# Performance work log

Hardware: AMD Instinct MI355X
Metric: run time of the kernel (lower is better)

The kernel has to match this reference:

```python
import jax, jax.numpy as jnp
import numpy as np

NUM_HEADS = 32
HEAD_DIM = 64  # C = 3 * NUM_HEADS * HEAD_DIM = 6144
SCALE = NUM_HEADS ** (-0.5)


def setup_inputs() -> dict:
    key = jax.random.key(0)
    B, N, C = 4, 4096, 3 * NUM_HEADS * HEAD_DIM
    x = jax.random.normal(key, (B, N, C), dtype=jnp.float32)
    return {"x": x}


def reference(x):
    B, N, C = x.shape
    # (B, N, 3, H, d) -> (3, B, H, N, d)
    qkv = x.reshape(B, N, 3, NUM_HEADS, HEAD_DIM).transpose(2, 0, 3, 1, 4)
    q, k, v = qkv[0], qkv[1], qkv[2]
    q = q * SCALE
    # kv = k^T @ v : (B, H, d, d)
    kv = jnp.einsum('bhnd,bhne->bhde', k, v)
    kv = jax.nn.softmax(kv, axis=-1)  # dropout p=0.0 -> identity
    # attn = q @ kv^T : (B, H, N, d)
    attn = jnp.einsum('bhnd,bhed->bhne', q, kv)
    # (B, H, N, d) -> (B, N, H*d)
    out = attn.transpose(0, 2, 1, 3).reshape(B, N, NUM_HEADS * HEAD_DIM)
    return out
```

## Files before the change

kernel.cpp:

```cpp
#include <hip/hip_runtime.h>
#include <math.h>


#define NN 4096
#define CC 6144
#define QSCALE 0.17677669529663687f
#define NCHUNK 8

typedef __attribute__((ext_vector_type(8))) short bf16x8;
typedef __attribute__((ext_vector_type(4))) float f32x4;

static __device__ __forceinline__ unsigned short f2bf(float f) {
  unsigned u = __float_as_uint(f);
  u = (u + 0x7FFFu + ((u >> 16) & 1u)) >> 16;
  return (unsigned short)u;
}

__global__ __launch_bounds__(256, 4) void k1_kv_accum(const float* __restrict__ x,
                                                      float* __restrict__ ws1) {
  __shared__ float lds[2][4096];

  const int bid = blockIdx.x;
  const int bh = bid >> 3;
  const int chunk = bid & (NCHUNK - 1);
  const int b = bh >> 5, h = bh & 31;
  const int t = threadIdx.x;
  const int lane = t & 63;
  const int w = t >> 6;

  const long long row0 = (long long)b * NN + (long long)chunk * 512;
  const float* kbase = x + row0 * CC + 2048 + h * 64;
  const float* kl = kbase + (lane & 3) * CC + (lane >> 2) + w * 16;
  const float* vl = kl + 2048;

#define K1_STAGE(sb, bbv)                                                                 \
  do {                                                                                    \
    const float* kp_ = kl + (sb) * 32 * CC;                                               \
    const float* vp_ = vl + (sb) * 32 * CC;                                               \
    _Pragma("unroll") for (int r_ = 0; r_ < 2; ++r_)                                      \
    _Pragma("unroll") for (int sub_ = 0; sub_ < 4; ++sub_) {                              \
      const int ro_ = (sub_ * 8 + r_ * 4) * CC;                                           \
      const int li_ = w * 512 + r_ * 256 + sub_ * 64;                                     \
      __builtin_amdgcn_global_load_lds(                                                   \
          (const __attribute__((address_space(1))) void*)(kp_ + ro_),                     \
          (__attribute__((address_space(3))) void*)&lds[(bbv)][li_], 4, 0, 0);            \
      __builtin_amdgcn_global_load_lds(                                                   \
          (const __attribute__((address_space(1))) void*)(vp_ + ro_),                     \
          (__attribute__((address_space(3))) void*)&lds[(bbv)][2048 + li_], 4, 0, 0);     \
    }                                                                                     \
  } while (0)

#define K1_FRAG(bbv, baseidx, hi8, lo8)                                                   \
  do {                                                                                    \
    const float4 f0_ = *(const float4*)&lds[(bbv)][(baseidx) + lane * 4];                 \
    const float4 f1_ = *(const float4*)&lds[(bbv)][(baseidx) + 256 + lane * 4];           \
    const float ff_[8] = {f0_.x, f0_.y, f0_.z, f0_.w, f1_.x, f1_.y, f1_.z, f1_.w};        \
    _Pragma("unroll") for (int e_ = 0; e_ < 8; ++e_) {                                    \
      const unsigned u_ = __float_as_uint(ff_[e_]);                                       \
      hi8[e_] = (short)(u_ >> 16);       \
      const float lof_ = ff_[e_] - __uint_as_float(u_ & 0xFFFF0000u);                     \
      lo8[e_] = (short)(__float_as_uint(lof_) >> 16);                                     \
    }                                                                                     \
  } while (0)

  f32x4 acc[2][2];
#pragma unroll
  for (int i2 = 0; i2 < 2; ++i2)
#pragma unroll
    for (int j2 = 0; j2 < 2; ++j2) acc[i2][j2] = (f32x4){0.f, 0.f, 0.f, 0.f};

  const int mt0 = (w & 1) * 2;
  const int nt0 = (w >> 1) * 2;

  K1_STAGE(0, 0);
  asm volatile("s_waitcnt vmcnt(0)" ::: "memory");
  __syncthreads();

  for (int s = 0; s < 16; ++s) {
    const int bb = s & 1;
    if (s + 1 < 16) K1_STAGE(s + 1, bb ^ 1);

    bf16x8 ah[2], al[2], bh8[2], bl8[2];
#pragma unroll
    for (int i2 = 0; i2 < 2; ++i2) K1_FRAG(bb, (mt0 + i2) * 512, ah[i2], al[i2]);
#pragma unroll
    for (int j2 = 0; j2 < 2; ++j2) K1_FRAG(bb, 2048 + (nt0 + j2) * 512, bh8[j2], bl8[j2]);

#pragma unroll
    for (int i2 = 0; i2 < 2; ++i2)
#pragma unroll
      for (int j2 = 0; j2 < 2; ++j2) {
        acc[i2][j2] = __builtin_amdgcn_mfma_f32_16x16x32_bf16(ah[i2], bh8[j2], acc[i2][j2], 0, 0, 0);
        acc[i2][j2] = __builtin_amdgcn_mfma_f32_16x16x32_bf16(ah[i2], bl8[j2], acc[i2][j2], 0, 0, 0);
        acc[i2][j2] = __builtin_amdgcn_mfma_f32_16x16x32_bf16(al[i2], bh8[j2], acc[i2][j2], 0, 0, 0);
      }

    if (s + 1 < 16) {
      asm volatile("s_waitcnt vmcnt(0)" ::: "memory");
      __syncthreads();
    }
  }

  float* dst = ws1 + (long long)bid * 4096;
  const int g = lane >> 4, cl = lane & 15;
#pragma unroll
  for (int i2 = 0; i2 < 2; ++i2)
#pragma unroll
    for (int j2 = 0; j2 < 2; ++j2)
#pragma unroll
      for (int r = 0; r < 4; ++r)
        dst[((mt0 + i2) * 16 + g * 4 + r) * 64 + (nt0 + j2) * 16 + cl] = acc[i2][j2][r];
}

__global__ __launch_bounds__(256) void k2_softmax(const float* __restrict__ ws1,
                                                  unsigned short* __restrict__ ws2bf) {
  const int bh = blockIdx.x;
  __shared__ float Cs[64 * 65];
  __shared__ float Ss[64 * 65];
  const int t = threadIdx.x;
  const float* src = ws1 + (long long)bh * NCHUNK * 4096;
  for (int s0 = t; s0 < 1024; s0 += 256) {
    float4 sum = {0.f, 0.f, 0.f, 0.f};
#pragma unroll
    for (int c = 0; c < NCHUNK; ++c) {
      const float4 f = *(const float4*)&src[c * 4096 + s0 * 4];
      sum.x += f.x; sum.y += f.y; sum.z += f.z; sum.w += f.w;
    }
    const float se[4] = {sum.x, sum.y, sum.z, sum.w};
#pragma unroll
    for (int e = 0; e < 4; ++e) {
      const int idx = s0 * 4 + e;
      Cs[(idx >> 6) * 65 + (idx & 63)] = se[e];
    }
  }
  __syncthreads();
  if (t < 64) {
    const int a = t;
    float m = -3.0e38f;
    for (int c = 0; c < 64; ++c) m = fmaxf(m, Cs[a * 65 + c]);
    float sum = 0.f;
    for (int c = 0; c < 64; ++c) {
      const float e = expf(Cs[a * 65 + c] - m);
      Ss[a * 65 + c] = e;
      sum += e;
    }
    const float inv = QSCALE / sum;
    for (int c = 0; c < 64; ++c) Ss[a * 65 + c] *= inv;
  }
  __syncthreads();
  unsigned short* dst = ws2bf + (long long)bh * 4096;
  for (int idx = t; idx < 4096; idx += 256) {
    const int j = idx >> 6;
    const int i = idx & 63;
    dst[idx] = f2bf(Ss[j * 65 + i]);
  }
}

__global__ __launch_bounds__(256) void k3_apply(const float* __restrict__ x,
                                                const unsigned short* __restrict__ ws2bf,
                                                float* __restrict__ out) {
  const int bid = blockIdx.x;
  const int b = bid >> 8;
  const int tile = bid & 255;
  const int t = threadIdx.x;
  const int lane = t & 63;
  const int w = t >> 6;
  const int bn = lane & 15;
  const int g = lane >> 4;

  const long long row = (long long)b * NN + tile * 16 + bn;
  const float* qrow = x + row * CC;
  float* orow = out + row * 2048;
  const unsigned short* sbase = ws2bf + (long long)b * 32 * 4096;

#pragma unroll 2
  for (int hh = 0; hh < 8; ++hh) {
    const int h = w * 8 + hh;
    const unsigned short* mb = sbase + h * 4096;

    bf16x8 afr[4][2];
#pragma unroll
    for (int mt = 0; mt < 4; ++mt)
#pragma unroll
      for (int kc = 0; kc < 2; ++kc)
        afr[mt][kc] = *(const bf16x8*)(mb + (mt * 16 + bn) * 64 + kc * 32 + g * 8);

    bf16x8 bfr[2];
#pragma unroll
    for (int kc = 0; kc < 2; ++kc) {
      const float* p = qrow + h * 64 + kc * 32 + g * 8;
      const float4 f0 = *(const float4*)p;
      const float4 f1 = *(const float4*)(p + 4);
      bf16x8 r;
      r[0] = (short)f2bf(f0.x); r[1] = (short)f2bf(f0.y);
      r[2] = (short)f2bf(f0.z); r[3] = (short)f2bf(f0.w);
      r[4] = (short)f2bf(f1.x); r[5] = (short)f2bf(f1.y);
      r[6] = (short)f2bf(f1.z); r[7] = (short)f2bf(f1.w);
      bfr[kc] = r;
    }

    f32x4 acc[4];
#pragma unroll
    for (int mt = 0; mt < 4; ++mt) acc[mt] = (f32x4){0.f, 0.f, 0.f, 0.f};
#pragma unroll
    for (int kc = 0; kc < 2; ++kc)
#pragma unroll
      for (int mt = 0; mt < 4; ++mt)
        acc[mt] = __builtin_amdgcn_mfma_f32_16x16x32_bf16(afr[mt][kc], bfr[kc], acc[mt], 0, 0, 0);

#pragma unroll
    for (int mt = 0; mt < 4; ++mt) {
      const float4 o = {acc[mt][0], acc[mt][1], acc[mt][2], acc[mt][3]};
      *(float4*)&orow[h * 64 + mt * 16 + g * 4] = o;
    }
  }
}

extern "C" void kernel_launch(void* const* d_in, const int* in_sizes, int n_in,
                              void* d_out, int out_size, void* d_ws, size_t ws_size,
                              hipStream_t stream) {
  const float* x = (const float*)d_in[0];
  float* out = (float*)d_out;
  float* ws1 = (float*)d_ws;
  unsigned short* ws2bf = (unsigned short*)(ws1 + (size_t)128 * NCHUNK * 4096);

  k1_kv_accum<<<128 * NCHUNK, 256, 0, stream>>>(x, ws1);
  k2_softmax<<<128, 256, 0, stream>>>(ws1, ws2bf);
  k3_apply<<<1024, 256, 0, stream>>>(x, ws2bf, out);
}
```

Measured before the change: 160.6 us.

## Restructure apply kernel per head-chunk with LDS double-buffered Q staging

The apply kernel's grid is remapped so each block handles one (batch, head, 512-row chunk). The bf16 softmax matrix is loaded into registers once per block instead of once per head iteration. Q rows are streamed into a double-buffered LDS region with global_load_lds, so the next stage's loads overlap the current MFMA work, and outputs are written with nontemporal stores. In exchange it adds LDS use, relies on per-wave vmcnt ordering instead of barriers, and uses 4-byte async loads, which may cut effective load bandwidth.

```diff
diff --git a/kernel.cpp b/kernel.cpp
--- a/kernel.cpp
+++ b/kernel.cpp
@@ -156,41 +156,57 @@
   }
 }
 
-__global__ __launch_bounds__(256) void k3_apply(const float* __restrict__ x,
-                                                const unsigned short* __restrict__ ws2bf,
-                                                float* __restrict__ out) {
+__global__ __launch_bounds__(256, 4) void k3_apply(const float* __restrict__ x,
+                                                   const unsigned short* __restrict__ ws2bf,
+                                                   float* __restrict__ out) {
+  __shared__ float qlds[2][4096];
+
   const int bid = blockIdx.x;
-  const int b = bid >> 8;
-  const int tile = bid & 255;
+  const int bh = bid >> 3;
+  const int chunk = bid & 7;
+  const int b = bh >> 5, h = bh & 31;
   const int t = threadIdx.x;
   const int lane = t & 63;
   const int w = t >> 6;
   const int bn = lane & 15;
   const int g = lane >> 4;
 
-  const long long row = (long long)b * NN + tile * 16 + bn;
-  const float* qrow = x + row * CC;
-  float* orow = out + row * 2048;
-  const unsigned short* sbase = ws2bf + (long long)b * 32 * 4096;
-
-#pragma unroll 2
-  for (int hh = 0; hh < 8; ++hh) {
-    const int h = w * 8 + hh;
-    const unsigned short* mb = sbase + h * 4096;
-
-    bf16x8 afr[4][2];
-#pragma unroll
-    for (int mt = 0; mt < 4; ++mt)
-#pragma unroll
-      for (int kc = 0; kc < 2; ++kc)
-        afr[mt][kc] = *(const bf16x8*)(mb + (mt * 16 + bn) * 64 + kc * 32 + g * 8);
+  const unsigned short* mb = ws2bf + (long long)bh * 4096;
+  bf16x8 afr[4][2];
+#pragma unroll
+  for (int mt = 0; mt < 4; ++mt)
+#pragma unroll
+    for (int kc = 0; kc < 2; ++kc)
+      afr[mt][kc] = *(const bf16x8*)(mb + (mt * 16 + bn) * 64 + kc * 32 + g * 8);
+
+  const long long row0 = (long long)b * NN + (long long)chunk * 512;
+  const float* ql = x + (row0 + (lane >> 2)) * CC + h * 64 + (lane & 3);
+
+#define K3_STAGE(sb, bbv)                                                                 \
+  do {                                                                                    \
+    const float* qp_ = ql + (long long)((sb) * 64 + w * 16) * CC;                         \
+    _Pragma("unroll") for (int m_ = 0; m_ < 16; ++m_) {                                   \
+      const int col_ = (m_ & 3) * 8 + ((m_ >> 2) & 1) * 4 + (m_ >> 3) * 32;               \
+      __builtin_amdgcn_global_load_lds(                                                   \
+          (const __attribute__((address_space(1))) void*)(qp_ + col_),                    \
+          (__attribute__((address_space(3))) void*)&qlds[(bbv)][w * 1024 + m_ * 64],      \
+          4, 0, 0);                                                                       \
+    }                                                                                     \
+  } while (0)
+
+  K3_STAGE(0, 0);
+  asm volatile("s_waitcnt vmcnt(0)" ::: "memory");
+
+  for (int s = 0; s < 8; ++s) {
+    const int bb = s & 1;
+    if (s + 1 < 8) K3_STAGE(s + 1, bb ^ 1);
 
     bf16x8 bfr[2];
 #pragma unroll
     for (int kc = 0; kc < 2; ++kc) {
-      const float* p = qrow + h * 64 + kc * 32 + g * 8;
-      const float4 f0 = *(const float4*)p;
-      const float4 f1 = *(const float4*)(p + 4);
+      const int base = w * 1024 + kc * 512;
+      const float4 f0 = *(const float4*)&qlds[bb][base + lane * 4];
+      const float4 f1 = *(const float4*)&qlds[bb][base + 256 + lane * 4];
       bf16x8 r;
       r[0] = (short)f2bf(f0.x); r[1] = (short)f2bf(f0.y);
       r[2] = (short)f2bf(f0.z); r[3] = (short)f2bf(f0.w);
@@ -208,10 +224,15 @@
       for (int mt = 0; mt < 4; ++mt)
         acc[mt] = __builtin_amdgcn_mfma_f32_16x16x32_bf16(afr[mt][kc], bfr[kc], acc[mt], 0, 0, 0);
 
+    const long long r = row0 + s * 64 + w * 16 + bn;
 #pragma unroll
     for (int mt = 0; mt < 4; ++mt) {
-      const float4 o = {acc[mt][0], acc[mt][1], acc[mt][2], acc[mt][3]};
-      *(float4*)&orow[h * 64 + mt * 16 + g * 4] = o;
+      f32x4* op = (f32x4*)(out + r * 2048 + h * 64 + mt * 16 + g * 4);
+      __builtin_nontemporal_store(acc[mt], op);
+    }
+
+    if (s + 1 < 8) {
+      asm volatile("s_waitcnt vmcnt(4)" ::: "memory");
     }
   }
 }
@@ -226,5 +247,5 @@
 
   k1_kv_accum<<<128 * NCHUNK, 256, 0, stream>>>(x, ws1);
   k2_softmax<<<128, 256, 0, stream>>>(ws1, ws2bf);
-  k3_apply<<<1024, 256, 0, stream>>>(x, ws2bf, out);
-}
+  k3_apply<<<128 * NCHUNK, 256, 0, stream>>>(x, ws2bf, out);
+}
```

Result: no change. 159.0 us (-1.0%).
